# Optimization experiments

Hardware: AMD Instinct MI355X
Metric: run time of the kernel (lower is better)

Reference implementation:

```python
import jax, jax.numpy as jnp
import numpy as np

HEADS = 8
HEAD_DIM = 32
SCALE = HEAD_DIM ** (-0.5)


def setup_inputs() -> dict:
    key = jax.random.key(0)
    k1, k2, k3 = jax.random.split(key, 3)
    B, DIM, N = 4, 512, 2048
    INNER = HEADS * HEAD_DIM  # 256
    x = jax.random.normal(k1, (B, DIM, N), dtype=jnp.float32)
    # Conv1d(kernel=1, bias=False) == channel-mixing matmul; weight (out_ch, in_ch)
    w_qkv = jax.random.normal(k2, (3 * INNER, DIM), dtype=jnp.float32) * (DIM ** -0.5)
    w_out = jax.random.normal(k3, (DIM, INNER), dtype=jnp.float32) * (INNER ** -0.5)
    b_out = jnp.zeros((DIM,), dtype=jnp.float32)
    return {"x": x, "w_qkv": w_qkv, "w_out": w_out, "b_out": b_out}


def reference(x, w_qkv, w_out, b_out):
    B, DIM, N = x.shape
    INNER = HEADS * HEAD_DIM
    # to_qkv: 1x1 conv over channels, then permute(0,2,1) -> (B, N, 3*INNER)
    qkv = jnp.einsum('bcn,oc->bno', x, w_qkv)
    q, k, v = jnp.split(qkv, 3, axis=-1)
    # 'b n (h d) -> b h n d'
    def to_heads(t):
        return t.reshape(B, N, HEADS, HEAD_DIM).transpose(0, 2, 1, 3)
    q, k, v = to_heads(q), to_heads(k), to_heads(v)
    # L2 similarity: -||q_i - k_j||_2 * scale, via expansion (avoids O(N^2 d) tensor)
    q2 = jnp.sum(q * q, axis=-1)            # (B,H,N)
    k2 = jnp.sum(k * k, axis=-1)            # (B,H,N)
    qk = jnp.einsum('bhid,bhjd->bhij', q, k)  # (B,H,N,N)
    dist2 = q2[..., :, None] + k2[..., None, :] - 2.0 * qk
    smi = -jnp.sqrt(jnp.maximum(dist2, 1e-12)) * SCALE
    attn = jax.nn.softmax(smi, axis=-1)
    out = jnp.einsum('bhij,bhjd->bhid', attn, v)  # (B,H,N,d)
    # 'b h n d -> b (h d) n'
    out = out.transpose(0, 1, 3, 2).reshape(B, INNER, N)
    # to_out: 1x1 conv with bias
    return jnp.einsum('bcn,oc->bon', out, w_out) + b_out[None, :, None]
```

## Files before the change

### kernel.cpp

```cpp
#include <hip/hip_runtime.h>
#include <math.h>

#define N_SEQ 2048
#define DIMC 512
#define INNER 256
#define C2F (0.17677669529663687f * 1.4426950408889634f)
#define C2F2 (C2F * C2F)

typedef short bf16x8 __attribute__((ext_vector_type(8)));
typedef float f32x4 __attribute__((ext_vector_type(4)));


static __device__ __forceinline__ ushort f2bf(float f) {
    uint x = __float_as_uint(f);
    x += 0x7fff + ((x >> 16) & 1);
    return (ushort)(x >> 16);
}
static __device__ __forceinline__ float bf2f(ushort u) {
    return __uint_as_float(((uint)u) << 16);
}
static __device__ __forceinline__ float fast_exp2_neg(float x) {
    float r; asm("v_exp_f32 %0, -%1" : "=v"(r) : "v"(x)); return r;
}
static __device__ __forceinline__ float fast_sqrt(float x) {
    float r; asm("v_sqrt_f32 %0, %1" : "=v"(r) : "v"(x)); return r;
}
static __device__ __forceinline__ void gload16(const void* g, void* l) {
    __builtin_amdgcn_global_load_lds(
        (const __attribute__((address_space(1))) void*)g,
        (__attribute__((address_space(3))) void*)l, 16, 0, 0);
}

__global__ void xpose_cvt(const float* __restrict__ x, ushort* __restrict__ xt) {
    __shared__ __align__(16) ushort T[64][72];
    const int b = blockIdx.z;
    const int c0 = blockIdx.y * 64;
    const int n0 = blockIdx.x * 64;
    const int t = threadIdx.x;
    const int cl = t >> 4;
    const int n4 = (t & 15) * 4;
    const float* xb = x + ((size_t)b * DIMC + c0) * N_SEQ + n0;
#pragma unroll
    for (int cc = 0; cc < 4; ++cc) {
        const int c = cl + cc * 16;
        float4 v = *(const float4*)(xb + (size_t)c * N_SEQ + n4);
        T[n4 + 0][c] = f2bf(v.x);
        T[n4 + 1][c] = f2bf(v.y);
        T[n4 + 2][c] = f2bf(v.z);
        T[n4 + 3][c] = f2bf(v.w);
    }
    __syncthreads();
    const int nl = t >> 2;
    const int c16 = (t & 3) * 16;
    uint4 v0 = *(const uint4*)&T[nl][c16];
    uint4 v1 = *(const uint4*)&T[nl][c16 + 8];
    ushort* dst = xt + ((size_t)b * N_SEQ + n0 + nl) * DIMC + c0 + c16;
    *(uint4*)dst = v0;
    *(uint4*)(dst + 8) = v1;
}

__global__ void wcvt2(const float* __restrict__ wq, const float* __restrict__ wo,
                      ushort* __restrict__ wq16, ushort* __restrict__ wo16) {
    const int bid = blockIdx.x;
    if (bid < 384) {
        int i = (bid * 256 + threadIdx.x) * 4;
        float4 v = *(const float4*)(wq + i);
        ushort4 p;
        p.x = f2bf(v.x); p.y = f2bf(v.y); p.z = f2bf(v.z); p.w = f2bf(v.w);
        *(ushort4*)(wq16 + i) = p;
    } else {
        int i = ((bid - 384) * 256 + threadIdx.x) * 4;
        float4 v = *(const float4*)(wo + i);
        ushort4 p;
        p.x = f2bf(v.x); p.y = f2bf(v.y); p.z = f2bf(v.z); p.w = f2bf(v.w);
        *(ushort4*)(wo16 + i) = p;
    }
}

__global__ __launch_bounds__(256) void qkv_mfma(const ushort* __restrict__ xt,
        const ushort* __restrict__ w16, ushort* __restrict__ ws16) {
    __shared__ __align__(16) ushort Wls[4 * 520];
    __shared__ __align__(16) ushort Xls[4 * 520];
    const int b = blockIdx.z;
    const int o0 = blockIdx.y * 64;
    const int n0 = blockIdx.x * 64;
    const int t = threadIdx.x;
    const int l = t & 63, w = t >> 6;
    const int q15 = l & 15, g = l >> 4;
    f32x4 acc[4];
#pragma unroll
    for (int nn = 0; nn < 4; ++nn) acc[nn] = (f32x4){0.f, 0.f, 0.f, 0.f};
    const int srow = t >> 2, sg = t & 3;
    const ushort* wsrc = w16 + (size_t)(o0 + srow) * DIMC + sg * 8;
    const ushort* xsrc = xt + ((size_t)b * N_SEQ + n0 + srow) * DIMC + sg * 8;
    uint4 wreg = *(const uint4*)wsrc;
    uint4 xreg = *(const uint4*)xsrc;
    for (int k0 = 0; k0 < DIMC; k0 += 32) {
        __builtin_amdgcn_s_barrier();
        __builtin_amdgcn_sched_barrier(0);
        *(uint4*)(Wls + sg * 520 + srow * 8) = wreg;
        *(uint4*)(Xls + sg * 520 + srow * 8) = xreg;
        if (k0 + 32 < DIMC) {
            wreg = *(const uint4*)(wsrc + k0 + 32);
            xreg = *(const uint4*)(xsrc + k0 + 32);
        }
        asm volatile("s_waitcnt lgkmcnt(0)" ::: "memory");
        __builtin_amdgcn_s_barrier();
        __builtin_amdgcn_sched_barrier(0);
        bf16x8 af = *(const bf16x8*)(Wls + g * 520 + (16 * w + q15) * 8);
        __builtin_amdgcn_s_setprio(1);
#pragma unroll
        for (int nn = 0; nn < 4; ++nn) {
            bf16x8 bfr = *(const bf16x8*)(Xls + g * 520 + (16 * nn + q15) * 8);
            acc[nn] = __builtin_amdgcn_mfma_f32_16x16x32_bf16(af, bfr, acc[nn], 0, 0, 0);
        }
        __builtin_amdgcn_s_setprio(0);
    }
    const int oatom = o0 + 16 * w;
    const int t_idx = oatom >> 8;
    const int h = (oatom >> 5) & 7;
    const int bh = b * 8 + h;
    const int d0 = (oatom & 31) + 4 * g;
    if (t_idx < 2) {
        ushort* dst = ws16 + (size_t)t_idx * 2097152 + (size_t)bh * 65536
                      + (size_t)(d0 >> 3) * 16384 + (d0 & 7);
#pragma unroll
        for (int nn = 0; nn < 4; ++nn) {
            const int n_ = n0 + 16 * nn + q15;
            ushort4 p;
            p.x = f2bf(acc[nn][0]); p.y = f2bf(acc[nn][1]);
            p.z = f2bf(acc[nn][2]); p.w = f2bf(acc[nn][3]);
            *(ushort4*)(dst + (size_t)n_ * 8) = p;
        }
    } else {
        ushort* dst = ws16 + (size_t)4194304 + (size_t)bh * 65536;
#pragma unroll
        for (int nn = 0; nn < 4; ++nn) {
            const int n_ = n0 + 16 * nn + q15;
            ushort* dd = dst + (size_t)(n_ >> 3) * 256 + (n_ & 7);
            dd[(d0 + 0) * 8] = f2bf(acc[nn][0]);
            dd[(d0 + 1) * 8] = f2bf(acc[nn][1]);
            dd[(d0 + 2) * 8] = f2bf(acc[nn][2]);
            dd[(d0 + 3) * 8] = f2bf(acc[nn][3]);
        }
    }
}

__global__ void sq_kernel(const ushort* __restrict__ ws16, float* __restrict__ k2) {
    const int idx = blockIdx.x * 256 + threadIdx.x;
    const int bh = idx >> 11, n = idx & 2047;
    const ushort* base = ws16 + 2097152 + (size_t)bh * 65536 + (size_t)n * 8;
    float s = 0.f;
#pragma unroll
    for (int g = 0; g < 4; ++g) {
        uint4 v = *(const uint4*)(base + (size_t)g * 16384);
        uint a[4] = {v.x, v.y, v.z, v.w};
#pragma unroll
        for (int e = 0; e < 4; ++e) {
            float lo = bf2f((ushort)(a[e] & 0xffff));
            float hi = bf2f((ushort)(a[e] >> 16));
            s += lo * lo + hi * hi;
        }
    }
    k2[idx] = s * (float)C2F2;
}

__global__ __launch_bounds__(256, 4) void attn_kernel(
        const ushort* __restrict__ ws16, const float* __restrict__ k2g,
        ushort* __restrict__ att16) {
    __shared__ __align__(16) ushort Kls[2 * 2048];
    __shared__ __align__(16) ushort Vls[2 * 2048];
    __shared__ __align__(16) float k2ls[2048];
    __shared__ __align__(16) ushort Pls[4][16][72];
    const int bid = blockIdx.x;
    const int sw = (bid & 7) * 128 + (bid >> 3);
    const int q0 = (sw & 31) * 64;
    const int bh = sw >> 5;
    const int b = bh >> 3, h = bh & 7;
    const int tid = threadIdx.x;
    const int l = tid & 63;
    const int w = tid >> 6;
    const int q15 = l & 15;
    const int g = l >> 4;
    const int qrow = q0 + 16 * w + q15;

    const ushort* Qbh = ws16 + (size_t)bh * 65536;
    const ushort* Kbh = ws16 + 2097152 + (size_t)bh * 65536;
    const ushort* Vbh = ws16 + 4194304 + (size_t)bh * 65536;
    const float* k2bh = k2g + (size_t)bh * 2048;

#define STAGE(T, BUF)                                                         \
    {                                                                         \
        const int j0s = (T) * 64;                                             \
        gload16(Kbh + (size_t)w * 16384 + (size_t)(j0s + l) * 8,              \
                Kls + (BUF) * 2048 + w * 512);                                \
        gload16(Vbh + (size_t)j0s * 32 + (size_t)w * 512 + (size_t)l * 8,     \
                Vls + (BUF) * 2048 + w * 512);                                \
    }

    gload16(k2bh + (size_t)(2 * w + 0) * 256 + (size_t)l * 4, k2ls + (2 * w + 0) * 256);
    gload16(k2bh + (size_t)(2 * w + 1) * 256 + (size_t)l * 4, k2ls + (2 * w + 1) * 256);
    STAGE(0, 0)

    const bf16x8 qf = *(const bf16x8*)(Qbh + (size_t)g * 16384 + (size_t)qrow * 8);
    float q2l = 0.f;
#pragma unroll
    for (int e = 0; e < 8; ++e) {
        float qe = bf2f((ushort)qf[e]);
        q2l = fmaf(qe, qe, q2l);
    }
    q2l += __shfl_xor(q2l, 16);
    q2l += __shfl_xor(q2l, 32);
    const float q2v = q2l * (float)C2F2;

    ushort* plane = &Pls[w][q15][0];
    f32x4 accO[2];
    accO[0] = (f32x4){0.f, 0.f, 0.f, 0.f};
    accO[1] = (f32x4){0.f, 0.f, 0.f, 0.f};
    float lsm = 0.f;

    asm volatile("s_waitcnt vmcnt(0)" ::: "memory");
    __builtin_amdgcn_s_barrier();
    __builtin_amdgcn_sched_barrier(0);

#define COMPUTE(T)                                                              \
    {                                                                           \
        const ushort* KlsP = Kls + ((T) & 1) * 2048;                            \
        const ushort* VlsP = Vls + ((T) & 1) * 2048;                            \
        const int jb = (T) * 64;                                                \
        bf16x8 kf[4];                                                           \
        _Pragma("unroll")                                                       \
        for (int k = 0; k < 4; ++k)                                             \
            kf[k] = *(const bf16x8*)(KlsP + g * 512 + (16 * k + q15) * 8);      \
        const f32x4 zz = (f32x4){0.f, 0.f, 0.f, 0.f};                           \
        f32x4 st[4];                                                            \
        __builtin_amdgcn_s_setprio(1);                                          \
        _Pragma("unroll")                                                       \
        for (int k = 0; k < 4; ++k)                                             \
            st[k] = __builtin_amdgcn_mfma_f32_16x16x32_bf16(kf[k], qf, zz, 0, 0, 0); \
        __builtin_amdgcn_s_setprio(0);                                          \
        float lt = 0.f;                                                         \
        _Pragma("unroll")                                                       \
        for (int k = 0; k < 4; ++k) {                                           \
            float4 kk = *(const float4*)(k2ls + jb + 16 * k + 4 * g);           \
            float ka[4] = {kk.x, kk.y, kk.z, kk.w};                             \
            float pr[4];                                                        \
            _Pragma("unroll")                                                   \
            for (int r = 0; r < 4; ++r) {                                       \
                float a = q2v + ka[r];                                          \
                float d2 = fmaf(-2.f * (float)C2F2, st[k][r], a);               \
                pr[r] = fast_exp2_neg(fast_sqrt(fmaxf(d2, 1e-12f)));            \
            }                                                                   \
            lt += (pr[0] + pr[1]) + (pr[2] + pr[3]);                            \
            uint pk0, pk1;                                                      \
            asm("v_cvt_pk_bf16_f32 %0, %1, %2" : "=v"(pk0) : "v"(pr[0]), "v"(pr[1])); \
            asm("v_cvt_pk_bf16_f32 %0, %1, %2" : "=v"(pk1) : "v"(pr[2]), "v"(pr[3])); \
            uint2 pv; pv.x = pk0; pv.y = pk1;                                   \
            *(uint2*)(plane + 16 * k + 4 * g) = pv;                             \
        }                                                                       \
        lsm += lt;                                                              \
        __builtin_amdgcn_s_setprio(1);                                          \
        _Pragma("unroll")                                                       \
        for (int jc = 0; jc < 2; ++jc) {                                        \
            bf16x8 pf = *(const bf16x8*)(plane + 32 * jc + 8 * g);              \
            _Pragma("unroll")                                                   \
            for (int dh = 0; dh < 2; ++dh) {                                    \
                bf16x8 vf = *(const bf16x8*)(VlsP + (4 * jc + g) * 256          \
                                             + (16 * dh + q15) * 8);            \
                accO[dh] = __builtin_amdgcn_mfma_f32_16x16x32_bf16(vf, pf, accO[dh], 0, 0, 0); \
            }                                                                   \
        }                                                                       \
        __builtin_amdgcn_s_setprio(0);                                          \
    }

#pragma unroll 1
    for (int t = 0; t < 31; ++t) {
        STAGE(t + 1, (t + 1) & 1)
        asm volatile("s_waitcnt vmcnt(2)" ::: "memory");
        __builtin_amdgcn_s_barrier();
        __builtin_amdgcn_sched_barrier(0);
        COMPUTE(t)
        __builtin_amdgcn_sched_barrier(0);
        __builtin_amdgcn_s_barrier();
    }
    asm volatile("s_waitcnt vmcnt(0)" ::: "memory");
    __builtin_amdgcn_s_barrier();
    __builtin_amdgcn_sched_barrier(0);
    COMPUTE(31)
#undef COMPUTE
#undef STAGE

    lsm += __shfl_xor(lsm, 16);
    lsm += __shfl_xor(lsm, 32);
    const float invl = 1.f / lsm;
    ushort* dst = att16 + ((size_t)(b * N_SEQ + qrow)) * INNER + h * 32 + 4 * g;
#pragma unroll
    for (int d = 0; d < 2; ++d) {
        ushort4 o;
        o.x = f2bf(accO[d][0] * invl); o.y = f2bf(accO[d][1] * invl);
        o.z = f2bf(accO[d][2] * invl); o.w = f2bf(accO[d][3] * invl);
        *(ushort4*)(dst + d * 16) = o;
    }
}

__global__ __launch_bounds__(256) void out_mfma(const ushort* __restrict__ att16,
        const ushort* __restrict__ wo16, const float* __restrict__ bias,
        float* __restrict__ out) {
    __shared__ __align__(16) ushort Wls[4 * 520];
    __shared__ __align__(16) ushort Als[4 * 520];
    const int b = blockIdx.z;
    const int o0 = blockIdx.y * 64;
    const int n0 = blockIdx.x * 64;
    const int t = threadIdx.x;
    const int l = t & 63, w = t >> 6;
    const int q15 = l & 15, g = l >> 4;
    f32x4 acc[4];
#pragma unroll
    for (int nn = 0; nn < 4; ++nn) acc[nn] = (f32x4){0.f, 0.f, 0.f, 0.f};
    const int srow = t >> 2, sg = t & 3;
    const ushort* wsrc = wo16 + (size_t)(o0 + srow) * INNER + sg * 8;
    const ushort* asrc = att16 + ((size_t)b * N_SEQ + n0 + srow) * INNER + sg * 8;
    uint4 wreg = *(const uint4*)wsrc;
    uint4 areg = *(const uint4*)asrc;
    for (int k0 = 0; k0 < INNER; k0 += 32) {
        __builtin_amdgcn_s_barrier();
        __builtin_amdgcn_sched_barrier(0);
        *(uint4*)(Wls + sg * 520 + srow * 8) = wreg;
        *(uint4*)(Als + sg * 520 + srow * 8) = areg;
        if (k0 + 32 < INNER) {
            wreg = *(const uint4*)(wsrc + k0 + 32);
            areg = *(const uint4*)(asrc + k0 + 32);
        }
        asm volatile("s_waitcnt lgkmcnt(0)" ::: "memory");
        __builtin_amdgcn_s_barrier();
        __builtin_amdgcn_sched_barrier(0);
        bf16x8 af = *(const bf16x8*)(Wls + g * 520 + (16 * w + q15) * 8);
        __builtin_amdgcn_s_setprio(1);
#pragma unroll
        for (int nn = 0; nn < 4; ++nn) {
            bf16x8 bfr = *(const bf16x8*)(Als + g * 520 + (16 * nn + q15) * 8);
            acc[nn] = __builtin_amdgcn_mfma_f32_16x16x32_bf16(af, bfr, acc[nn], 0, 0, 0);
        }
        __builtin_amdgcn_s_setprio(0);
    }
    const int obase = o0 + 16 * w + 4 * g;
    float4 bi = *(const float4*)(bias + obase);
    float* ob = out + ((size_t)b * DIMC + obase) * N_SEQ;
#pragma unroll
    for (int nn = 0; nn < 4; ++nn) {
        const int n_ = n0 + 16 * nn + q15;
        ob[0 * N_SEQ + n_] = acc[nn][0] + bi.x;
        ob[1 * N_SEQ + n_] = acc[nn][1] + bi.y;
        ob[2 * N_SEQ + n_] = acc[nn][2] + bi.z;
        ob[3 * N_SEQ + n_] = acc[nn][3] + bi.w;
    }
}

extern "C" void kernel_launch(void* const* d_in, const int* in_sizes, int n_in,
                              void* d_out, int out_size, void* d_ws, size_t ws_size,
                              hipStream_t stream) {
    const float* x = (const float*)d_in[0];
    const float* w_qkv = (const float*)d_in[1];
    const float* w_out = (const float*)d_in[2];
    const float* b_out = (const float*)d_in[3];
    ushort* ws16 = (ushort*)d_ws;
    float* k2f = (float*)((char*)d_ws + (12 << 20) + (256 << 10));
    ushort* att16 = (ushort*)((char*)d_ws + (13 << 20));
    ushort* xt16 = (ushort*)((char*)d_ws + (21 << 20));
    ushort* wq16 = (ushort*)((char*)d_ws + (29 << 20));
    ushort* wo16 = (ushort*)((char*)d_ws + (30 << 20));
    float* out = (float*)d_out;

    xpose_cvt<<<dim3(32, 8, 4), 256, 0, stream>>>(x, xt16);
    wcvt2<<<dim3(512), 256, 0, stream>>>(w_qkv, w_out, wq16, wo16);
    qkv_mfma<<<dim3(32, 12, 4), 256, 0, stream>>>(xt16, wq16, ws16);
    sq_kernel<<<dim3(256), 256, 0, stream>>>(ws16, k2f);
    attn_kernel<<<dim3(1024), 256, 0, stream>>>(ws16, k2f, att16);
    out_mfma<<<dim3(32, 8, 4), 256, 0, stream>>>(att16, wo16, b_out, out);
}
```

Measured before the change: 89.06 us.

## Merge prep kernels, XOR-swizzle K/V LDS tiles, stream k2 per tile

Fuses the x transpose/convert and weight-convert kernels into one launch to remove a kernel boundary. In the attention kernel, K and V tiles are loaded into LDS with XOR-swizzled row positions, and the reads apply the matching swizzle, to cut LDS bank conflicts. The full per-head k2 preload is replaced by a per-tile 64-float double-buffered load, which shrinks LDS use. Pls padding also changes. The extra k2 load per stage requires a different vmcnt wait count, and the swizzle must match exactly between writer and reader.

```diff
diff --git a/kernel.cpp b/kernel.cpp
--- a/kernel.cpp
+++ b/kernel.cpp
@@ -30,46 +30,53 @@
         (const __attribute__((address_space(1))) void*)g,
         (__attribute__((address_space(3))) void*)l, 16, 0, 0);
 }
-
-__global__ void xpose_cvt(const float* __restrict__ x, ushort* __restrict__ xt) {
+static __device__ __forceinline__ void gload4(const void* g, void* l) {
+    __builtin_amdgcn_global_load_lds(
+        (const __attribute__((address_space(1))) void*)g,
+        (__attribute__((address_space(3))) void*)l, 4, 0, 0);
+}
+
+__global__ void prep_kernel(const float* __restrict__ x,
+                            const float* __restrict__ wq,
+                            const float* __restrict__ wo,
+                            ushort* __restrict__ xt,
+                            ushort* __restrict__ wq16,
+                            ushort* __restrict__ wo16) {
     __shared__ __align__(16) ushort T[64][72];
-    const int b = blockIdx.z;
-    const int c0 = blockIdx.y * 64;
-    const int n0 = blockIdx.x * 64;
+    const int bid = blockIdx.x;
     const int t = threadIdx.x;
-    const int cl = t >> 4;
-    const int n4 = (t & 15) * 4;
-    const float* xb = x + ((size_t)b * DIMC + c0) * N_SEQ + n0;
-#pragma unroll
-    for (int cc = 0; cc < 4; ++cc) {
-        const int c = cl + cc * 16;
-        float4 v = *(const float4*)(xb + (size_t)c * N_SEQ + n4);
-        T[n4 + 0][c] = f2bf(v.x);
-        T[n4 + 1][c] = f2bf(v.y);
-        T[n4 + 2][c] = f2bf(v.z);
-        T[n4 + 3][c] = f2bf(v.w);
-    }
-    __syncthreads();
-    const int nl = t >> 2;
-    const int c16 = (t & 3) * 16;
-    uint4 v0 = *(const uint4*)&T[nl][c16];
-    uint4 v1 = *(const uint4*)&T[nl][c16 + 8];
-    ushort* dst = xt + ((size_t)b * N_SEQ + n0 + nl) * DIMC + c0 + c16;
-    *(uint4*)dst = v0;
-    *(uint4*)(dst + 8) = v1;
-}
-
-__global__ void wcvt2(const float* __restrict__ wq, const float* __restrict__ wo,
-                      ushort* __restrict__ wq16, ushort* __restrict__ wo16) {
-    const int bid = blockIdx.x;
-    if (bid < 384) {
-        int i = (bid * 256 + threadIdx.x) * 4;
+    if (bid < 1024) {
+        const int n0 = (bid & 31) * 64;
+        const int c0 = ((bid >> 5) & 7) * 64;
+        const int b = bid >> 8;
+        const int cl = t >> 4;
+        const int n4 = (t & 15) * 4;
+        const float* xb = x + ((size_t)b * DIMC + c0) * N_SEQ + n0;
+#pragma unroll
+        for (int cc = 0; cc < 4; ++cc) {
+            const int c = cl + cc * 16;
+            float4 v = *(const float4*)(xb + (size_t)c * N_SEQ + n4);
+            T[n4 + 0][c] = f2bf(v.x);
+            T[n4 + 1][c] = f2bf(v.y);
+            T[n4 + 2][c] = f2bf(v.z);
+            T[n4 + 3][c] = f2bf(v.w);
+        }
+        __syncthreads();
+        const int nl = t >> 2;
+        const int c16 = (t & 3) * 16;
+        uint4 v0 = *(const uint4*)&T[nl][c16];
+        uint4 v1 = *(const uint4*)&T[nl][c16 + 8];
+        ushort* dst = xt + ((size_t)b * N_SEQ + n0 + nl) * DIMC + c0 + c16;
+        *(uint4*)dst = v0;
+        *(uint4*)(dst + 8) = v1;
+    } else if (bid < 1408) {
+        int i = ((bid - 1024) * 256 + t) * 4;
         float4 v = *(const float4*)(wq + i);
         ushort4 p;
         p.x = f2bf(v.x); p.y = f2bf(v.y); p.z = f2bf(v.z); p.w = f2bf(v.w);
         *(ushort4*)(wq16 + i) = p;
     } else {
-        int i = ((bid - 384) * 256 + threadIdx.x) * 4;
+        int i = ((bid - 1408) * 256 + t) * 4;
         float4 v = *(const float4*)(wo + i);
         ushort4 p;
         p.x = f2bf(v.x); p.y = f2bf(v.y); p.z = f2bf(v.z); p.w = f2bf(v.w);
@@ -170,8 +177,8 @@
         ushort* __restrict__ att16) {
     __shared__ __align__(16) ushort Kls[2 * 2048];
     __shared__ __align__(16) ushort Vls[2 * 2048];
-    __shared__ __align__(16) float k2ls[2048];
-    __shared__ __align__(16) ushort Pls[4][16][72];
+    __shared__ __align__(16) float k2ls[2 * 64];
+    __shared__ __align__(16) ushort Pls[4][16][140];
     const int bid = blockIdx.x;
     const int sw = (bid & 7) * 128 + (bid >> 3);
     const int q0 = (sw & 31) * 64;
@@ -183,6 +190,10 @@
     const int q15 = l & 15;
     const int g = l >> 4;
     const int qrow = q0 + 16 * w + q15;
+    const int q15xg = q15 ^ g;
+    const int lxw = l ^ w;
+    const int vc = 2 * w + (l >> 5);
+    const int vsw = (l & 31) ^ (vc & 7);
 
     const ushort* Qbh = ws16 + (size_t)bh * 65536;
     const ushort* Kbh = ws16 + 2097152 + (size_t)bh * 65536;
@@ -192,14 +203,13 @@
 #define STAGE(T, BUF)                                                         \
     {                                                                         \
         const int j0s = (T) * 64;                                             \
-        gload16(Kbh + (size_t)w * 16384 + (size_t)(j0s + l) * 8,              \
+        gload16(Kbh + (size_t)w * 16384 + (size_t)(j0s + lxw) * 8,            \
                 Kls + (BUF) * 2048 + w * 512);                                \
-        gload16(Vbh + (size_t)j0s * 32 + (size_t)w * 512 + (size_t)l * 8,     \
+        gload16(Vbh + (size_t)j0s * 32 + (size_t)vc * 256 + (size_t)vsw * 8,  \
                 Vls + (BUF) * 2048 + w * 512);                                \
-    }
-
-    gload16(k2bh + (size_t)(2 * w + 0) * 256 + (size_t)l * 4, k2ls + (2 * w + 0) * 256);
-    gload16(k2bh + (size_t)(2 * w + 1) * 256 + (size_t)l * 4, k2ls + (2 * w + 1) * 256);
+        gload4(k2bh + j0s + l, k2ls + (BUF) * 64);                            \
+    }
+
     STAGE(0, 0)
 
     const bf16x8 qf = *(const bf16x8*)(Qbh + (size_t)g * 16384 + (size_t)qrow * 8);
@@ -227,11 +237,11 @@
     {                                                                           \
         const ushort* KlsP = Kls + ((T) & 1) * 2048;                            \
         const ushort* VlsP = Vls + ((T) & 1) * 2048;                            \
-        const int jb = (T) * 64;                                                \
+        const float* k2P = k2ls + ((T) & 1) * 64;                               \
         bf16x8 kf[4];                                                           \
         _Pragma("unroll")                                                       \
         for (int k = 0; k < 4; ++k)                                             \
-            kf[k] = *(const bf16x8*)(KlsP + g * 512 + (16 * k + q15) * 8);      \
+            kf[k] = *(const bf16x8*)(KlsP + g * 512 + (16 * k + q15xg) * 8);    \
         const f32x4 zz = (f32x4){0.f, 0.f, 0.f, 0.f};                           \
         f32x4 st[4];                                                            \
         __builtin_amdgcn_s_setprio(1);                                          \
@@ -242,7 +252,7 @@
         float lt = 0.f;                                                         \
         _Pragma("unroll")                                                       \
         for (int k = 0; k < 4; ++k) {                                           \
-            float4 kk = *(const float4*)(k2ls + jb + 16 * k + 4 * g);           \
+            float4 kk = *(const float4*)(k2P + 16 * k + 4 * g);                 \
             float ka[4] = {kk.x, kk.y, kk.z, kk.w};                             \
             float pr[4];                                                        \
             _Pragma("unroll")                                                   \
@@ -266,7 +276,7 @@
             _Pragma("unroll")                                                   \
             for (int dh = 0; dh < 2; ++dh) {                                    \
                 bf16x8 vf = *(const bf16x8*)(VlsP + (4 * jc + g) * 256          \
-                                             + (16 * dh + q15) * 8);            \
+                                 + (16 * dh + (q15xg ^ (jc << 2))) * 8);        \
                 accO[dh] = __builtin_amdgcn_mfma_f32_16x16x32_bf16(vf, pf, accO[dh], 0, 0, 0); \
             }                                                                   \
         }                                                                       \
@@ -276,7 +286,7 @@
 #pragma unroll 1
     for (int t = 0; t < 31; ++t) {
         STAGE(t + 1, (t + 1) & 1)
-        asm volatile("s_waitcnt vmcnt(2)" ::: "memory");
+        asm volatile("s_waitcnt vmcnt(3)" ::: "memory");
         __builtin_amdgcn_s_barrier();
         __builtin_amdgcn_sched_barrier(0);
         COMPUTE(t)
@@ -371,8 +381,7 @@
     ushort* wo16 = (ushort*)((char*)d_ws + (30 << 20));
     float* out = (float*)d_out;
 
-    xpose_cvt<<<dim3(32, 8, 4), 256, 0, stream>>>(x, xt16);
-    wcvt2<<<dim3(512), 256, 0, stream>>>(w_qkv, w_out, wq16, wo16);
+    prep_kernel<<<dim3(1536), 256, 0, stream>>>(x, w_qkv, w_out, xt16, wq16, wo16);
     qkv_mfma<<<dim3(32, 12, 4), 256, 0, stream>>>(xt16, wq16, ws16);
     sq_kernel<<<dim3(256), 256, 0, stream>>>(ws16, k2f);
     attn_kernel<<<dim3(1024), 256, 0, stream>>>(ws16, k2f, att16);
```

Measured after the change: 103.5 us. +16.2%, slower.
